# Kernel optimization log

Measured on AMD Instinct MI355X. Metric: run time of the kernel, lower is better.

## Reference

```python
import jax, jax.numpy as jnp
import numpy as np

B, S, H, D = 32, 2048, 1024, 1024  # batch, src seq len, hidden_dim, output_dim


def setup_inputs() -> dict:
    key = jax.random.key(0)
    k1, k2, k3, k4, k5 = jax.random.split(key, 5)
    hidden = jax.random.normal(k1, (B, H), dtype=jnp.float32)
    encoder_outs = jax.random.normal(k2, (B, S, D), dtype=jnp.float32)
    src_lens = jax.random.randint(k3, (B,), 1, S + 1, dtype=jnp.int32)
    src_lens = src_lens.at[0].set(S)  # ensure max(src_lens) == S (matches torch max_len)
    W1 = jax.random.normal(k4, (D, H), dtype=jnp.float32) * (1.0 / np.sqrt(H))
    W2 = jax.random.normal(k5, (D, H + D), dtype=jnp.float32) * (1.0 / np.sqrt(H + D))
    return {"hidden": hidden, "encoder_outs": encoder_outs, "src_lens": src_lens,
            "W1": W1, "W2": W2}


def reference(hidden, encoder_outs, src_lens, W1, W2):
    # x = l1(hidden): [B, D]
    x = hidden @ W1.T
    # unfused QK dot-product: att_score [B, S] (torch keeps it [S, B]; we use batch-first)
    att = jnp.einsum('bsd,bd->bs', encoder_outs, x)
    # length mask [B, S]
    mask = jnp.arange(S, dtype=src_lens.dtype)[None, :] < src_lens[:, None]
    masked = jnp.where(mask, att, 0.0)
    # faithful to original quirk: any exact-zero entry (masked OR genuinely zero score)
    # is replaced with -1e10 before softmax
    masked = jnp.where(masked == 0.0, jnp.float32(-1e10), masked)
    attn = jax.nn.softmax(masked, axis=1)  # softmax over source positions
    # weighted sum of encoder outputs: [B, D]
    ctx = jnp.einsum('bs,bsd->bd', attn, encoder_outs)
    out = jnp.tanh(jnp.concatenate([ctx, hidden], axis=1) @ W2.T)
    # original returns attn_scores with shape [S, B]
    return out, attn.T
```

## Files before the change

kernel.cpp:

```cpp
#include <hip/hip_runtime.h>

namespace {
constexpr int kB = 32;
constexpr int kS = 2048;
constexpr int kH = 1024;
constexpr int kD = 1024;
constexpr int kK2 = kH + kD;
constexpr float kWThresh = 1e-8f;

typedef float f32x4 __attribute__((ext_vector_type(4)));

__device__ inline float waveReduceSum(float v) {
#pragma unroll
  for (int off = 32; off > 0; off >>= 1) v += __shfl_down(v, off, 64);
  return v;
}
__device__ inline float waveReduceMax(float v) {
#pragma unroll
  for (int off = 32; off > 0; off >>= 1) v = fmaxf(v, __shfl_down(v, off, 64));
  return v;
}
}

__global__ __launch_bounds__(256) void k_gemv1(const float* __restrict__ hidden,
                                               const float* __restrict__ W1,
                                               float* __restrict__ x) {
  const int wid = blockIdx.x * 4 + (threadIdx.x >> 6);
  const int lane = threadIdx.x & 63;
  const int n0 = (wid & 511) * 2;
  const int b0 = (wid >> 9) * 8;
  const f32x4* w0v = (const f32x4*)(W1 + (size_t)n0 * kH) + lane;
  const f32x4* w1v = (const f32x4*)(W1 + (size_t)(n0 + 1) * kH) + lane;
  f32x4 w0[4], w1[4];
#pragma unroll
  for (int i = 0; i < 4; ++i) { w0[i] = w0v[64 * i]; w1[i] = w1v[64 * i]; }
  for (int b = b0; b < b0 + 8; ++b) {
    const f32x4* hv = (const f32x4*)(hidden + (size_t)b * kH) + lane;
    f32x4 s0v = {0.f, 0.f, 0.f, 0.f}, s1v = {0.f, 0.f, 0.f, 0.f};
#pragma unroll
    for (int i = 0; i < 4; ++i) {
      const f32x4 h = hv[64 * i];
      s0v += w0[i] * h;
      s1v += w1[i] * h;
    }
    const float a0 = waveReduceSum(s0v.x + s0v.y + s0v.z + s0v.w);
    const float a1 = waveReduceSum(s1v.x + s1v.y + s1v.z + s1v.w);
    if (lane == 0) {
      x[(size_t)b * kD + n0] = a0;
      x[(size_t)b * kD + n0 + 1] = a1;
    }
  }
}

__global__ __launch_bounds__(256) void k_att(const float* __restrict__ enc,
                                             const float* __restrict__ x,
                                             const int* __restrict__ lens,
                                             float* __restrict__ att) {
  const int lane = threadIdx.x & 63;
  const int wib = threadIdx.x >> 6;
  const int b = blockIdx.x & 31;
  const int s0 = (blockIdx.x >> 5) * 16 + wib * 4;
  const int len = lens[b];
  if (s0 >= len) return;
  const f32x4* xv = (const f32x4*)(x + (size_t)b * kD) + lane;
  f32x4 xr[4];
#pragma unroll
  for (int i = 0; i < 4; ++i) xr[i] = xv[64 * i];
  float acc[4];
#pragma unroll
  for (int r = 0; r < 4; ++r) {
    const f32x4* ev = (const f32x4*)(enc + ((size_t)b * kS + s0 + r) * kD) + lane;
    f32x4 d = {0.f, 0.f, 0.f, 0.f};
#pragma unroll
    for (int i = 0; i < 4; ++i) {
      const f32x4 e = ev[64 * i];
      d += e * xr[i];
    }
    acc[r] = waveReduceSum(d.x + d.y + d.z + d.w);
  }
  if (lane == 0) {
    f32x4 o;
    o.x = acc[0]; o.y = acc[1]; o.z = acc[2]; o.w = acc[3];
    *(f32x4*)(att + (size_t)b * kS + s0) = o;
  }
}

__global__ __launch_bounds__(256) void k_smout(const float* __restrict__ att,
                                               const int* __restrict__ lens,
                                               const float* __restrict__ enc,
                                               const float* __restrict__ hidden,
                                               const float* __restrict__ W2,
                                               float* __restrict__ attnT,
                                               float* __restrict__ out) {
  const int b = blockIdx.x >> 4;
  const int sub = ((blockIdx.x & 7) << 1) | ((blockIdx.x >> 3) & 1);
  const int t = threadIdx.x;
  const int lane = t & 63;
  const int wib = t >> 6;
  const int len = lens[b];
  __shared__ float sred[4];
  __shared__ float swts[kS];
  __shared__ int sidx[kS];
  __shared__ int scount;
  __shared__ float ctx_lds[kD];

  float v[8];
#pragma unroll
  for (int i = 0; i < 8; ++i) {
    const int s = t + i * 256;
    float a = -1e10f;
    if (s < len) {
      const float av = att[(size_t)b * kS + s];
      a = (av == 0.0f) ? -1e10f : av;
    }
    v[i] = a;
  }
  float m = v[0];
#pragma unroll
  for (int i = 1; i < 8; ++i) m = fmaxf(m, v[i]);
  m = waveReduceMax(m);
  if (lane == 0) sred[wib] = m;
  __syncthreads();
  m = fmaxf(fmaxf(sred[0], sred[1]), fmaxf(sred[2], sred[3]));
  __syncthreads();
  float p[8];
  float sum = 0.f;
#pragma unroll
  for (int i = 0; i < 8; ++i) {
    p[i] = __expf(v[i] - m);
    sum += p[i];
  }
  sum = waveReduceSum(sum);
  if (lane == 0) sred[wib] = sum;
  __syncthreads();
  const float inv = 1.0f / (sred[0] + sred[1] + sred[2] + sred[3]);
  if (t == 0) scount = 0;
  __syncthreads();
#pragma unroll
  for (int i = 0; i < 8; ++i) {
    const int s = t + i * 256;
    const float w = p[i] * inv;
    if (sub == 0) attnT[(size_t)s * kB + b] = w;
    if (w > kWThresh) {
      const int k = atomicAdd(&scount, 1);
      sidx[k] = s;
      swts[k] = w;
    }
  }
  __syncthreads();

  const int n = scount;
  const float* ebase = enc + (size_t)b * kS * kD + t;
  float acc0 = 0.f, acc1 = 0.f, acc2 = 0.f, acc3 = 0.f;
  for (int k = 0; k < n; ++k) {
    const float w = swts[k];
    const float* row = ebase + (size_t)sidx[k] * kD;
    acc0 += w * row[0];
    acc1 += w * row[256];
    acc2 += w * row[512];
    acc3 += w * row[768];
  }
  ctx_lds[t] = acc0;
  ctx_lds[t + 256] = acc1;
  ctx_lds[t + 512] = acc2;
  ctx_lds[t + 768] = acc3;
  __syncthreads();

  f32x4 c[8];
  const f32x4* cl = (const f32x4*)ctx_lds + lane;
  const f32x4* hl = (const f32x4*)(hidden + (size_t)b * kH) + lane;
#pragma unroll
  for (int i = 0; i < 4; ++i) c[i] = cl[64 * i];
#pragma unroll
  for (int i = 0; i < 4; ++i) c[i + 4] = hl[64 * i];
#pragma unroll
  for (int j = 0; j < 8; ++j) {
    const int n0 = sub * 64 + wib * 16 + j * 2;
    const f32x4* w0v = (const f32x4*)(W2 + (size_t)n0 * kK2) + lane;
    const f32x4* w1v = (const f32x4*)(W2 + (size_t)(n0 + 1) * kK2) + lane;
    f32x4 s0v = {0.f, 0.f, 0.f, 0.f}, s1v = {0.f, 0.f, 0.f, 0.f};
#pragma unroll
    for (int i = 0; i < 8; ++i) {
      s0v += w0v[64 * i] * c[i];
      s1v += w1v[64 * i] * c[i];
    }
    const float a0 = waveReduceSum(s0v.x + s0v.y + s0v.z + s0v.w);
    const float a1 = waveReduceSum(s1v.x + s1v.y + s1v.z + s1v.w);
    if (lane == 0) {
      out[(size_t)b * kD + n0] = tanhf(a0);
      out[(size_t)b * kD + n0 + 1] = tanhf(a1);
    }
  }
}

extern "C" void kernel_launch(void* const* d_in, const int* in_sizes, int n_in,
                              void* d_out, int out_size, void* d_ws, size_t ws_size,
                              hipStream_t stream) {
  const float* hidden = (const float*)d_in[0];
  const float* enc    = (const float*)d_in[1];
  const int*   lens   = (const int*)d_in[2];
  const float* W1     = (const float*)d_in[3];
  const float* W2     = (const float*)d_in[4];

  float* out   = (float*)d_out;
  float* attnT = out + (size_t)kB * kD;

  float* ws  = (float*)d_ws;
  float* x   = ws;
  float* att = ws + 32768;

  k_gemv1<<<512, 256, 0, stream>>>(hidden, W1, x);
  k_att<<<kB * (kS / 16), 256, 0, stream>>>(enc, x, lens, att);
  k_smout<<<kB * 16, 256, 0, stream>>>(att, lens, enc, hidden, W2, attnT, out);
}
```

Baseline: 58.94 us.

## Precompute hidden half of output GEMV inside attention-score kernel

Result: no change. 59.51 us (+1.0%).

```diff
diff --git a/kernel.cpp b/kernel.cpp
--- a/kernel.cpp
+++ b/kernel.cpp
@@ -7,6 +7,7 @@
 constexpr int kD = 1024;
 constexpr int kK2 = kH + kD;
 constexpr float kWThresh = 1e-8f;
+constexpr int kAttBlocks = kB * (kS / 16);
 
 typedef float f32x4 __attribute__((ext_vector_type(4)));
 
@@ -52,14 +53,47 @@
   }
 }
 
-__global__ __launch_bounds__(256) void k_att(const float* __restrict__ enc,
-                                             const float* __restrict__ x,
-                                             const int* __restrict__ lens,
-                                             float* __restrict__ att) {
+__global__ __launch_bounds__(256) void k_attpb(const float* __restrict__ enc,
+                                               const float* __restrict__ x,
+                                               const int* __restrict__ lens,
+                                               const float* __restrict__ hidden,
+                                               const float* __restrict__ W2,
+                                               float* __restrict__ att,
+                                               float* __restrict__ pb) {
   const int lane = threadIdx.x & 63;
   const int wib = threadIdx.x >> 6;
+
+  if (blockIdx.x >= kAttBlocks) {
+    const int wid = (blockIdx.x - kAttBlocks) * 4 + wib;
+    const int n0 = (wid & 511) * 2;
+    const int b0 = (wid >> 9) * 8;
+    const f32x4* w0v = (const f32x4*)(W2 + (size_t)n0 * kK2 + kH) + lane;
+    const f32x4* w1v = (const f32x4*)(W2 + (size_t)(n0 + 1) * kK2 + kH) + lane;
+    f32x4 w0[4], w1[4];
+#pragma unroll
+    for (int i = 0; i < 4; ++i) { w0[i] = w0v[64 * i]; w1[i] = w1v[64 * i]; }
+    for (int b = b0; b < b0 + 8; ++b) {
+      const f32x4* hv = (const f32x4*)(hidden + (size_t)b * kH) + lane;
+      f32x4 s0v = {0.f, 0.f, 0.f, 0.f}, s1v = {0.f, 0.f, 0.f, 0.f};
+#pragma unroll
+      for (int i = 0; i < 4; ++i) {
+        const f32x4 h = hv[64 * i];
+        s0v += w0[i] * h;
+        s1v += w1[i] * h;
+      }
+      const float a0 = waveReduceSum(s0v.x + s0v.y + s0v.z + s0v.w);
+      const float a1 = waveReduceSum(s1v.x + s1v.y + s1v.z + s1v.w);
+      if (lane == 0) {
+        pb[(size_t)b * kD + n0] = a0;
+        pb[(size_t)b * kD + n0 + 1] = a1;
+      }
+    }
+    return;
+  }
+
   const int b = blockIdx.x & 31;
-  const int s0 = (blockIdx.x >> 5) * 16 + wib * 4;
+  const int c = ((blockIdx.x >> 5) * 85) & 127;
+  const int s0 = c * 16 + wib * 4;
   const int len = lens[b];
   if (s0 >= len) return;
   const f32x4* xv = (const f32x4*)(x + (size_t)b * kD) + lane;
@@ -88,7 +122,7 @@
 __global__ __launch_bounds__(256) void k_smout(const float* __restrict__ att,
                                                const int* __restrict__ lens,
                                                const float* __restrict__ enc,
-                                               const float* __restrict__ hidden,
+                                               const float* __restrict__ pb,
                                                const float* __restrict__ W2,
                                                float* __restrict__ attnT,
                                                float* __restrict__ out) {
@@ -166,13 +200,10 @@
   ctx_lds[t + 768] = acc3;
   __syncthreads();
 
-  f32x4 c[8];
+  f32x4 c[4];
   const f32x4* cl = (const f32x4*)ctx_lds + lane;
-  const f32x4* hl = (const f32x4*)(hidden + (size_t)b * kH) + lane;
 #pragma unroll
   for (int i = 0; i < 4; ++i) c[i] = cl[64 * i];
-#pragma unroll
-  for (int i = 0; i < 4; ++i) c[i + 4] = hl[64 * i];
 #pragma unroll
   for (int j = 0; j < 8; ++j) {
     const int n0 = sub * 64 + wib * 16 + j * 2;
@@ -180,15 +211,15 @@
     const f32x4* w1v = (const f32x4*)(W2 + (size_t)(n0 + 1) * kK2) + lane;
     f32x4 s0v = {0.f, 0.f, 0.f, 0.f}, s1v = {0.f, 0.f, 0.f, 0.f};
 #pragma unroll
-    for (int i = 0; i < 8; ++i) {
+    for (int i = 0; i < 4; ++i) {
       s0v += w0v[64 * i] * c[i];
       s1v += w1v[64 * i] * c[i];
     }
     const float a0 = waveReduceSum(s0v.x + s0v.y + s0v.z + s0v.w);
     const float a1 = waveReduceSum(s1v.x + s1v.y + s1v.z + s1v.w);
     if (lane == 0) {
-      out[(size_t)b * kD + n0] = tanhf(a0);
-      out[(size_t)b * kD + n0 + 1] = tanhf(a1);
+      out[(size_t)b * kD + n0] = tanhf(a0 + pb[(size_t)b * kD + n0]);
+      out[(size_t)b * kD + n0 + 1] = tanhf(a1 + pb[(size_t)b * kD + n0 + 1]);
     }
   }
 }
@@ -208,8 +239,9 @@
   float* ws  = (float*)d_ws;
   float* x   = ws;
   float* att = ws + 32768;
+  float* pb  = ws + 98304;
 
   k_gemv1<<<512, 256, 0, stream>>>(hidden, W1, x);
-  k_att<<<kB * (kS / 16), 256, 0, stream>>>(enc, x, lens, att);
-  k_smout<<<kB * 16, 256, 0, stream>>>(att, lens, enc, hidden, W2, attnT, out);
-}
+  k_attpb<<<kAttBlocks + 512, 256, 0, stream>>>(enc, x, lens, hidden, W2, att, pb);
+  k_smout<<<kB * 16, 256, 0, stream>>>(att, lens, enc, pb, W2, attnT, out);
+}
```
